# Performance work log

Hardware: AMD Instinct MI355X
Metric: run time of the kernel (lower is better)

Reference implementation:

```python
import jax, jax.numpy as jnp
import numpy as np

B, T, E, H = 256, 256, 384, 64

def setup_inputs() -> dict:
    key = jax.random.key(0)
    ks = jax.random.split(key, 4)
    s = 1.0 / np.sqrt(E)
    return {
        "x":  jax.random.normal(ks[0], (B, T, E), dtype=jnp.float32),
        "Wq": jax.random.normal(ks[1], (E, H), dtype=jnp.float32) * s,
        "bq": jnp.zeros((H,), dtype=jnp.float32),
        "Wk": jax.random.normal(ks[2], (E, H), dtype=jnp.float32) * s,
        "bk": jnp.zeros((H,), dtype=jnp.float32),
        "Wv": jax.random.normal(ks[3], (E, H), dtype=jnp.float32) * s,
        "bv": jnp.zeros((H,), dtype=jnp.float32),
    }

def reference(x, Wq, bq, Wk, bk, Wv, bv):
    # QKV projections: [B,T,E] @ [E,H] -> [B,T,H]
    q = x @ Wq + bq
    k = x @ Wk + bk
    v = x @ Wv + bv
    # attention scores (NOTE: original has no 1/sqrt(d) scaling)
    wei = jnp.einsum('bth,bsh->bts', q, k)  # [B,T,T]
    causal = jnp.tril(jnp.ones((T, T), dtype=bool))
    wei = jnp.where(causal, wei, -jnp.inf)
    wei = jax.nn.softmax(wei, axis=-1)
    # dropout is identity in eval mode
    out = jnp.einsum('bts,bsh->bth', wei, v)  # [B,T,H]
    return out
```

## Files before the change

### kernel.cpp

```cpp
#include <hip/hip_runtime.h>
#include <math.h>

#define Bb 256
#define Tt 256
#define Ee 384
#define Hh 64

typedef __attribute__((ext_vector_type(8))) short bf16x8;
typedef __attribute__((ext_vector_type(4))) float f32x4;
typedef __attribute__((ext_vector_type(4))) unsigned int u32x4;

__device__ inline short f2bf(float f) {
    unsigned u = __float_as_uint(f);
    u += 0x7FFFu + ((u >> 16) & 1);
    return (short)(u >> 16);
}
__device__ inline float bf2f(short s) {
    return __uint_as_float(((unsigned)(unsigned short)s) << 16);
}
__device__ inline unsigned cvt_pk_bf16(float a, float b) {
    unsigned r;
    asm("v_cvt_pk_bf16_f32 %0, %1, %2" : "=v"(r) : "v"(a), "v"(b));
    return r;
}

#define MFMA16(a, b, c) __builtin_amdgcn_mfma_f32_16x16x32_bf16((a), (b), (c), 0, 0, 0)

#define WLO_OFF 147456

#define BB0 65536
#define K_HI 0
#define K_LO 32768
#define VF   65536
#define QH   98304
#define QL   116736
#define PBASE 98304
#define SMEM_BYTES 135168

__global__ __launch_bounds__(256) void prep_w(
    const float* __restrict__ Wq, const float* __restrict__ Wk,
    const float* __restrict__ Wv, unsigned char* __restrict__ wsp)
{
    int u = blockIdx.x * 256 + threadIdx.x;
    if (u >= 9216) return;
    int frag = u >> 6;
    int lu   = u & 63;
    int ec   = frag / 12, tct = frag - ec * 12;
    int koct = lu >> 4, n = lu & 15;
    int col  = tct * 16 + n;
    const float* Wm = (col < 64) ? Wq : ((col < 128) ? Wk : Wv);
    int c = col & 63;
    bf16x8 hi8, lo8;
    #pragma unroll
    for (int j = 0; j < 8; ++j) {
        float v = Wm[(ec * 32 + koct * 8 + j) * 64 + c];
        short h = f2bf(v);
        hi8[j] = h;
        lo8[j] = f2bf(v - bf2f(h));
    }
    *reinterpret_cast<bf16x8*>(wsp + frag * 1024 + lu * 16) = hi8;
    *reinterpret_cast<bf16x8*>(wsp + WLO_OFF + frag * 1024 + lu * 16) = lo8;
}

__global__ __launch_bounds__(1024) void head_fused(
    const float* __restrict__ x,
    const float* __restrict__ bq, const float* __restrict__ bk,
    const float* __restrict__ bv,
    const unsigned char* __restrict__ wsp,
    float* __restrict__ out)
{
    __shared__ __align__(16) unsigned char smem[SMEM_BYTES];

    const int b    = blockIdx.x;
    const int tid  = threadIdx.x;
    const int w    = tid >> 6;
    const int lane = tid & 63;
    const int quad = lane >> 4;
    const int nl   = lane & 15;
    const int ri   = w >> 2;
    const int cj   = w & 3;

    f32x4 acc[4][3];
    #pragma unroll
    for (int i = 0; i < 4; ++i)
        #pragma unroll
        for (int j = 0; j < 3; ++j) acc[i][j] = (f32x4){0,0,0,0};

    const float4* x4 = reinterpret_cast<const float4*>(x + (size_t)b * Tt * Ee);

    auto bgld = [&](int ecn) {
        if (w < 12) {
            int p = ecn & 1;
            const unsigned char* ghi = wsp + (size_t)(ecn * 12 + w) * 1024 + (size_t)lane * 16;
            const unsigned char* glo = ghi + WLO_OFF;
            __builtin_amdgcn_global_load_lds(
                (const __attribute__((address_space(1))) unsigned*)ghi,
                (__attribute__((address_space(3))) unsigned*)(smem + BB0 + p * 24576 + w * 1024),
                16, 0, 0);
            __builtin_amdgcn_global_load_lds(
                (const __attribute__((address_space(1))) unsigned*)glo,
                (__attribute__((address_space(3))) unsigned*)(smem + BB0 + p * 24576 + 12288 + w * 1024),
                16, 0, 0);
        }
    };

    const int pt = tid & 255;
    const float4* xp = x4 + pt * 96;
    unsigned char* adst = smem + (pt >> 4) * 1024 + (pt & 15) * 16;
    float4 px[8];

    auto loadX = [&](int ecsrc) {
        const float4* xr_ = xp + ecsrc * 8;
        #pragma unroll
        for (int j = 0; j < 8; ++j) px[j] = xr_[j];
    };
    auto stageWrite = [&](int nb) {
        #pragma unroll
        for (int ko = 0; ko < 4; ++ko) {
            float v0 = px[2*ko+0].x, v1 = px[2*ko+0].y,
                  v2 = px[2*ko+0].z, v3 = px[2*ko+0].w,
                  v4 = px[2*ko+1].x, v5 = px[2*ko+1].y,
                  v6 = px[2*ko+1].z, v7 = px[2*ko+1].w;
            unsigned h0 = cvt_pk_bf16(v0, v1);
            unsigned h1 = cvt_pk_bf16(v2, v3);
            unsigned h2 = cvt_pk_bf16(v4, v5);
            unsigned h3 = cvt_pk_bf16(v6, v7);
            unsigned l0 = cvt_pk_bf16(v0 - __uint_as_float(h0 << 16),
                                      v1 - __uint_as_float(h0 & 0xFFFF0000u));
            unsigned l1 = cvt_pk_bf16(v2 - __uint_as_float(h1 << 16),
                                      v3 - __uint_as_float(h1 & 0xFFFF0000u));
            unsigned l2 = cvt_pk_bf16(v4 - __uint_as_float(h2 << 16),
                                      v5 - __uint_as_float(h2 & 0xFFFF0000u));
            unsigned l3 = cvt_pk_bf16(v6 - __uint_as_float(h3 << 16),
                                      v7 - __uint_as_float(h3 & 0xFFFF0000u));
            u32x4 hv = {h0, h1, h2, h3};
            u32x4 lv = {l0, l1, l2, l3};
            *reinterpret_cast<u32x4*>(adst + nb + ko * 256) = hv;
            *reinterpret_cast<u32x4*>(adst + nb + 16384 + ko * 256) = lv;
        }
    };

    bgld(0);
    if (w >= 12) {
        loadX(0);
        stageWrite(0);
        loadX(1);
    }

    for (int ec = 0; ec < 12; ++ec) {
        __syncthreads();
        if (w < 12) {
            if (ec < 11) bgld(ec + 1);
        } else {
            if (ec < 11) stageWrite((1 - (ec & 1)) * 32768);
            if (ec < 10) loadX(ec + 2);
        }

        const int ab = (ec & 1) * 32768;
        const int bb = BB0 + (ec & 1) * 24576;
        bf16x8 bh[3], bl[3];
        #pragma unroll
        for (int ct = 0; ct < 3; ++ct) {
            int o = bb + (cj * 3 + ct) * 1024 + lane * 16;
            bh[ct] = *reinterpret_cast<bf16x8*>(smem + o);
            bl[ct] = *reinterpret_cast<bf16x8*>(smem + o + 12288);
        }
        __builtin_amdgcn_s_setprio(1);
        #pragma unroll
        for (int rt = 0; rt < 4; ++rt) {
            int ao = ab + (4 * ri + rt) * 1024 + lane * 16;
            bf16x8 ah = *reinterpret_cast<bf16x8*>(smem + ao);
            bf16x8 al = *reinterpret_cast<bf16x8*>(smem + ao + 16384);
            #pragma unroll
            for (int ct = 0; ct < 3; ++ct) {
                acc[rt][ct] = MFMA16(ah, bh[ct], acc[rt][ct]);
                acc[rt][ct] = MFMA16(al, bh[ct], acc[rt][ct]);
                acc[rt][ct] = MFMA16(ah, bl[ct], acc[rt][ct]);
            }
        }
        __builtin_amdgcn_s_setprio(0);
    }
    __syncthreads();

    #pragma unroll
    for (int ct = 0; ct < 3; ++ct) {
        int col = (cj * 3 + ct) * 16 + nl;
        float bias = (col < 64) ? bq[col] : (col < 128 ? bk[col - 64] : bv[col - 128]);
        #pragma unroll
        for (int rt = 0; rt < 4; ++rt)
            #pragma unroll
            for (int r = 0; r < 4; ++r) acc[rt][ct][r] += bias;
    }

    #pragma unroll
    for (int ct = 0; ct < 3; ++ct) {
        int col = (cj * 3 + ct) * 16 + nl;
        #pragma unroll
        for (int rt = 0; rt < 4; ++rt) {
            #pragma unroll
            for (int r = 0; r < 4; ++r) {
                float val = acc[rt][ct][r];
                int s = ri * 64 + rt * 16 + quad * 4 + r;
                if (col >= 64 && col < 128) {
                    int h = col - 64;
                    int addr = ((s >> 4) * 2 + (h >> 5)) * 1024
                             + ((((h & 31) >> 3) * 16 + (s & 15)) * 8 + (h & 7)) * 2;
                    short hi = f2bf(val);
                    short lo = f2bf(val - bf2f(hi));
                    *reinterpret_cast<short*>(smem + K_HI + addr) = hi;
                    *reinterpret_cast<short*>(smem + K_LO + addr) = lo;
                } else if (col >= 128) {
                    int h = col - 128, sl = s & 31;
                    int addr = ((s >> 5) * 4 + (h >> 4)) * 1024
                             + (((sl >> 3) * 16 + (h & 15)) * 8 + (sl & 7)) * 2;
                    *reinterpret_cast<short*>(smem + VF + addr) = f2bf(val);
                }
            }
        }
    }

    auto writeQhalf = [&]() {
        #pragma unroll
        for (int ct = 0; ct < 3; ++ct) {
            int col = (cj * 3 + ct) * 16 + nl;
            if (col < 64) {
                #pragma unroll
                for (int rt = 0; rt < 4; ++rt) {
                    #pragma unroll
                    for (int r = 0; r < 4; ++r) {
                        float val = acc[rt][ct][r];
                        int s = ri * 64 + rt * 16 + quad * 4 + r;
                        int rloc = s & 127;
                        short hi = f2bf(val);
                        short lo = f2bf(val - bf2f(hi));
                        *reinterpret_cast<short*>(smem + QH + (rloc * 72 + col) * 2) = hi;
                        *reinterpret_cast<short*>(smem + QL + (rloc * 72 + col) * 2) = lo;
                    }
                }
            }
        }
    };
    bf16x8 qh0, qh1, ql0, ql1;
    auto readQ = [&]() {
        int rloc = (16 * w + nl) & 127;
        int base = rloc * 144;
        qh0 = *reinterpret_cast<bf16x8*>(smem + QH + base + quad * 16);
        qh1 = *reinterpret_cast<bf16x8*>(smem + QH + base + 64 + quad * 16);
        ql0 = *reinterpret_cast<bf16x8*>(smem + QL + base + quad * 16);
        ql1 = *reinterpret_cast<bf16x8*>(smem + QL + base + 64 + quad * 16);
    };

    if (ri < 2) writeQhalf();
    __syncthreads();
    if (w < 8) readQ();
    __syncthreads();
    if (ri >= 2) writeQhalf();
    __syncthreads();
    if (w >= 8) readQ();
    __syncthreads();

    f32x4 oacc[4];
    #pragma unroll
    for (int i = 0; i < 4; ++i) oacc[i] = (f32x4){0,0,0,0};
    float lsum4[4] = {0.f, 0.f, 0.f, 0.f};
    const int t0 = w * 16;
    unsigned char* pb = smem + PBASE + w * 1344;
    const int npairs = (w >> 1) + 1;

    for (int p = 0; p < npairs; ++p) {
        float rs[4] = {0.f, 0.f, 0.f, 0.f};
        #pragma unroll
        for (int hf = 0; hf < 2; ++hf) {
            int st = 2 * p + hf;
            f32x4 s0 = (f32x4){0,0,0,0}, s1 = (f32x4){0,0,0,0};
            int kb = st * 2048 + lane * 16;
            bf16x8 kh0 = *reinterpret_cast<bf16x8*>(smem + K_HI + kb);
            bf16x8 kh1 = *reinterpret_cast<bf16x8*>(smem + K_HI + kb + 1024);
            bf16x8 kl0 = *reinterpret_cast<bf16x8*>(smem + K_LO + kb);
            bf16x8 kl1 = *reinterpret_cast<bf16x8*>(smem + K_LO + kb + 1024);
            __builtin_amdgcn_s_setprio(1);
            s0 = MFMA16(qh0, kh0, s0);
            s1 = MFMA16(qh1, kh1, s1);
            s0 = MFMA16(ql0, kh0, s0);
            s1 = MFMA16(ql1, kh1, s1);
            s0 = MFMA16(qh0, kl0, s0);
            s1 = MFMA16(qh1, kl1, s1);
            __builtin_amdgcn_s_setprio(0);
            int sg = st * 16 + nl;
            #pragma unroll
            for (int r = 0; r < 4; ++r) {
                int tg = t0 + quad * 4 + r;
                float sv = s0[r] + s1[r];
                float pv = (sg <= tg) ? __expf(sv) : 0.f;
                rs[r] += pv;
                *reinterpret_cast<short*>(pb + ((quad * 4 + r) * 40 + hf * 16 + nl) * 2) = f2bf(pv);
            }
        }
        #pragma unroll
        for (int r = 0; r < 4; ++r) {
            float v = rs[r];
            v += __shfl_xor(v, 1);
            v += __shfl_xor(v, 2);
            v += __shfl_xor(v, 4);
            v += __shfl_xor(v, 8);
            lsum4[r] += v;
        }
        asm volatile("s_waitcnt lgkmcnt(0)" ::: "memory");
        bf16x8 pa = *reinterpret_cast<bf16x8*>(pb + (nl * 40 + quad * 8) * 2);
        int vb = p * 4096 + lane * 16;
        __builtin_amdgcn_s_setprio(1);
        #pragma unroll
        for (int nt = 0; nt < 4; ++nt) {
            bf16x8 vf = *reinterpret_cast<bf16x8*>(smem + VF + vb + nt * 1024);
            oacc[nt] = MFMA16(pa, vf, oacc[nt]);
        }
        __builtin_amdgcn_s_setprio(0);
    }

    float* ob = out + (size_t)b * Tt * Hh + (size_t)t0 * Hh;
    #pragma unroll
    for (int r = 0; r < 4; ++r) {
        float inv = 1.0f / lsum4[r];
        #pragma unroll
        for (int nt = 0; nt < 4; ++nt)
            ob[(quad * 4 + r) * 64 + nt * 16 + nl] = oacc[nt][r] * inv;
    }
}

extern "C" void kernel_launch(void* const* d_in, const int* in_sizes, int n_in,
                              void* d_out, int out_size, void* d_ws, size_t ws_size,
                              hipStream_t stream) {
    const float* x  = (const float*)d_in[0];
    const float* Wq = (const float*)d_in[1];
    const float* bq = (const float*)d_in[2];
    const float* Wk = (const float*)d_in[3];
    const float* bk = (const float*)d_in[4];
    const float* Wv = (const float*)d_in[5];
    const float* bv = (const float*)d_in[6];
    float* out = (float*)d_out;
    unsigned char* wsp = (unsigned char*)d_ws;
    hipLaunchKernelGGL(prep_w, dim3(36), dim3(256), 0, stream, Wq, Wk, Wv, wsp);
    hipLaunchKernelGGL(head_fused, dim3(Bb), dim3(1024), 0, stream,
                       x, bq, bk, bv, wsp, out);
}
```

Measured before the change: 188.1 us.

## Prefetch next K tiles and interleave score MFMAs; stage weight prep through LDS

The attention loop now computes both 16-column score subtiles in one interleaved MFMA sequence, giving two independent accumulation chains where there was one. It also loads the V fragments early and prefetches the next pair's K hi/lo fragments into registers before the PV MFMAs, so LDS latency overlaps with compute. The explicit lgkmcnt wait is replaced by a compiler memory barrier. Separately, the weight prep kernel stages each 32x64 weight slab in shared memory so its global reads are coalesced. The cost is higher register pressure from keeping eight K fragments and four V fragments live.

```diff
diff --git a/kernel.cpp b/kernel.cpp
--- a/kernel.cpp
+++ b/kernel.cpp
@@ -41,23 +41,32 @@
     const float* __restrict__ Wq, const float* __restrict__ Wk,
     const float* __restrict__ Wv, unsigned char* __restrict__ wsp)
 {
-    int u = blockIdx.x * 256 + threadIdx.x;
-    if (u >= 9216) return;
-    int frag = u >> 6;
-    int lu   = u & 63;
-    int ec   = frag / 12, tct = frag - ec * 12;
-    int koct = lu >> 4, n = lu & 15;
-    int col  = tct * 16 + n;
-    const float* Wm = (col < 64) ? Wq : ((col < 128) ? Wk : Wv);
-    int c = col & 63;
+    __shared__ float wlds[32 * 66];
+    const int bid = blockIdx.x;
+    const int ec  = bid / 3, m = bid - ec * 3;
+    const float* Wm = (m == 0) ? Wq : (m == 1 ? Wk : Wv);
+    const int tid = threadIdx.x;
+
+    const float4* src = reinterpret_cast<const float4*>(Wm + ec * 2048) + tid * 2;
+    float4 a = src[0], b = src[1];
+    int f = tid * 8;
+    float* d = wlds + (f >> 6) * 66 + (f & 63);
+    d[0] = a.x; d[1] = a.y; d[2] = a.z; d[3] = a.w;
+    d[4] = b.x; d[5] = b.y; d[6] = b.z; d[7] = b.w;
+    __syncthreads();
+
+    const int tl = tid >> 6, lu = tid & 63;
+    const int koct = lu >> 4, n = lu & 15;
+    const int c = tl * 16 + n;
     bf16x8 hi8, lo8;
     #pragma unroll
     for (int j = 0; j < 8; ++j) {
-        float v = Wm[(ec * 32 + koct * 8 + j) * 64 + c];
+        float v = wlds[(koct * 8 + j) * 66 + c];
         short h = f2bf(v);
         hi8[j] = h;
         lo8[j] = f2bf(v - bf2f(h));
     }
+    const int frag = ec * 12 + m * 4 + tl;
     *reinterpret_cast<bf16x8*>(wsp + frag * 1024 + lu * 16) = hi8;
     *reinterpret_cast<bf16x8*>(wsp + WLO_OFF + frag * 1024 + lu * 16) = lo8;
 }
@@ -267,35 +276,54 @@
     unsigned char* pb = smem + PBASE + w * 1344;
     const int npairs = (w >> 1) + 1;
 
+    bf16x8 kA0, kA1, kA2, kA3, kB0, kB1, kB2, kB3;
+#define LDK(P) do {                                                     \
+        int kb0_ = (2 * (P)) * 2048 + lane * 16;                        \
+        kA0 = *reinterpret_cast<bf16x8*>(smem + K_HI + kb0_);           \
+        kA1 = *reinterpret_cast<bf16x8*>(smem + K_HI + kb0_ + 1024);    \
+        kA2 = *reinterpret_cast<bf16x8*>(smem + K_LO + kb0_);           \
+        kA3 = *reinterpret_cast<bf16x8*>(smem + K_LO + kb0_ + 1024);    \
+        kB0 = *reinterpret_cast<bf16x8*>(smem + K_HI + kb0_ + 2048);    \
+        kB1 = *reinterpret_cast<bf16x8*>(smem + K_HI + kb0_ + 3072);    \
+        kB2 = *reinterpret_cast<bf16x8*>(smem + K_LO + kb0_ + 2048);    \
+        kB3 = *reinterpret_cast<bf16x8*>(smem + K_LO + kb0_ + 3072);    \
+    } while (0)
+
+    LDK(0);
     for (int p = 0; p < npairs; ++p) {
-        float rs[4] = {0.f, 0.f, 0.f, 0.f};
-        #pragma unroll
-        for (int hf = 0; hf < 2; ++hf) {
-            int st = 2 * p + hf;
-            f32x4 s0 = (f32x4){0,0,0,0}, s1 = (f32x4){0,0,0,0};
-            int kb = st * 2048 + lane * 16;
-            bf16x8 kh0 = *reinterpret_cast<bf16x8*>(smem + K_HI + kb);
-            bf16x8 kh1 = *reinterpret_cast<bf16x8*>(smem + K_HI + kb + 1024);
-            bf16x8 kl0 = *reinterpret_cast<bf16x8*>(smem + K_LO + kb);
-            bf16x8 kl1 = *reinterpret_cast<bf16x8*>(smem + K_LO + kb + 1024);
-            __builtin_amdgcn_s_setprio(1);
-            s0 = MFMA16(qh0, kh0, s0);
-            s1 = MFMA16(qh1, kh1, s1);
-            s0 = MFMA16(ql0, kh0, s0);
-            s1 = MFMA16(ql1, kh1, s1);
-            s0 = MFMA16(qh0, kl0, s0);
-            s1 = MFMA16(qh1, kl1, s1);
-            __builtin_amdgcn_s_setprio(0);
-            int sg = st * 16 + nl;
-            #pragma unroll
-            for (int r = 0; r < 4; ++r) {
-                int tg = t0 + quad * 4 + r;
-                float sv = s0[r] + s1[r];
-                float pv = (sg <= tg) ? __expf(sv) : 0.f;
-                rs[r] += pv;
-                *reinterpret_cast<short*>(pb + ((quad * 4 + r) * 40 + hf * 16 + nl) * 2) = f2bf(pv);
-            }
-        }
+        f32x4 sa0 = (f32x4){0,0,0,0}, sa1 = (f32x4){0,0,0,0};
+        f32x4 sb0 = (f32x4){0,0,0,0}, sb1 = (f32x4){0,0,0,0};
+        __builtin_amdgcn_s_setprio(1);
+        sa0 = MFMA16(qh0, kA0, sa0);  sb0 = MFMA16(qh0, kB0, sb0);
+        sa1 = MFMA16(qh1, kA1, sa1);  sb1 = MFMA16(qh1, kB1, sb1);
+        sa0 = MFMA16(ql0, kA0, sa0);  sb0 = MFMA16(ql0, kB0, sb0);
+        sa1 = MFMA16(ql1, kA1, sa1);  sb1 = MFMA16(ql1, kB1, sb1);
+        sa0 = MFMA16(qh0, kA2, sa0);  sb0 = MFMA16(qh0, kB2, sb0);
+        sa1 = MFMA16(qh1, kA3, sa1);  sb1 = MFMA16(qh1, kB3, sb1);
+        __builtin_amdgcn_s_setprio(0);
+
+        float rs[4];
+        const int sg0 = 32 * p + nl, sg1 = sg0 + 16;
+        #pragma unroll
+        for (int r = 0; r < 4; ++r) {
+            int tg = t0 + quad * 4 + r;
+            float sva = sa0[r] + sa1[r];
+            float svb = sb0[r] + sb1[r];
+            float pva = (sg0 <= tg) ? __expf(sva) : 0.f;
+            float pvb = (sg1 <= tg) ? __expf(svb) : 0.f;
+            rs[r] = pva + pvb;
+            *reinterpret_cast<short*>(pb + ((quad * 4 + r) * 40 + nl) * 2)      = f2bf(pva);
+            *reinterpret_cast<short*>(pb + ((quad * 4 + r) * 40 + 16 + nl) * 2) = f2bf(pvb);
+        }
+        asm volatile("" ::: "memory");
+        bf16x8 pa  = *reinterpret_cast<bf16x8*>(pb + (nl * 40 + quad * 8) * 2);
+        int vb = p * 4096 + lane * 16;
+        bf16x8 vf0 = *reinterpret_cast<bf16x8*>(smem + VF + vb);
+        bf16x8 vf1 = *reinterpret_cast<bf16x8*>(smem + VF + vb + 1024);
+        bf16x8 vf2 = *reinterpret_cast<bf16x8*>(smem + VF + vb + 2048);
+        bf16x8 vf3 = *reinterpret_cast<bf16x8*>(smem + VF + vb + 3072);
+        if (p + 1 < npairs) LDK(p + 1);
+
         #pragma unroll
         for (int r = 0; r < 4; ++r) {
             float v = rs[r];
@@ -305,17 +333,14 @@
             v += __shfl_xor(v, 8);
             lsum4[r] += v;
         }
-        asm volatile("s_waitcnt lgkmcnt(0)" ::: "memory");
-        bf16x8 pa = *reinterpret_cast<bf16x8*>(pb + (nl * 40 + quad * 8) * 2);
-        int vb = p * 4096 + lane * 16;
         __builtin_amdgcn_s_setprio(1);
-        #pragma unroll
-        for (int nt = 0; nt < 4; ++nt) {
-            bf16x8 vf = *reinterpret_cast<bf16x8*>(smem + VF + vb + nt * 1024);
-            oacc[nt] = MFMA16(pa, vf, oacc[nt]);
-        }
+        oacc[0] = MFMA16(pa, vf0, oacc[0]);
+        oacc[1] = MFMA16(pa, vf1, oacc[1]);
+        oacc[2] = MFMA16(pa, vf2, oacc[2]);
+        oacc[3] = MFMA16(pa, vf3, oacc[3]);
         __builtin_amdgcn_s_setprio(0);
     }
+#undef LDK
 
     float* ob = out + (size_t)b * Tt * Hh + (size_t)t0 * Hh;
     #pragma unroll
```

Result: no change. 188.3 us (+0.1%).
